# Kernel optimization log

Hardware: AMD Instinct MI355X
Metric: run time of the kernel (lower is better)

The kernel has to match this reference:

```python
import jax, jax.numpy as jnp
import numpy as np

EMBED_DIM = 1024
NUM_HEADS = 16
HEAD_DIM = EMBED_DIM // NUM_HEADS
B, S = 4, 2048


def setup_inputs() -> dict:
    key = jax.random.key(0)
    ks = jax.random.split(key, 9)
    s = 1.0 / np.sqrt(EMBED_DIM)
    x = jax.random.normal(ks[0], (B, S, EMBED_DIM), dtype=jnp.float32)
    # nn.Linear weights stored [out, in]; y = x @ W.T + b
    Wq = jax.random.uniform(ks[1], (EMBED_DIM, EMBED_DIM), jnp.float32, -s, s)
    bq = jax.random.uniform(ks[2], (EMBED_DIM,), jnp.float32, -s, s)
    Wk = jax.random.uniform(ks[3], (EMBED_DIM, EMBED_DIM), jnp.float32, -s, s)
    bk = jax.random.uniform(ks[4], (EMBED_DIM,), jnp.float32, -s, s)
    Wv = jax.random.uniform(ks[5], (EMBED_DIM, EMBED_DIM), jnp.float32, -s, s)
    bv = jax.random.uniform(ks[6], (EMBED_DIM,), jnp.float32, -s, s)
    Wo = jax.random.uniform(ks[7], (EMBED_DIM, EMBED_DIM), jnp.float32, -s, s)
    bo = jax.random.uniform(ks[8], (EMBED_DIM,), jnp.float32, -s, s)
    return {"x": x, "Wq": Wq, "bq": bq, "Wk": Wk, "bk": bk,
            "Wv": Wv, "bv": bv, "Wo": Wo, "bo": bo}


def _split_heads(t):
    b, s, _ = t.shape
    return t.reshape(b, s, NUM_HEADS, HEAD_DIM).transpose(0, 2, 1, 3)  # [B,H,S,D]


def reference(x, Wq, bq, Wk, bk, Wv, bv, Wo, bo):
    q = _split_heads(x @ Wq.T + bq)
    k = _split_heads(x @ Wk.T + bk)
    v = _split_heads(x @ Wv.T + bv)
    scores = jnp.einsum('bhqd,bhkd->bhqk', q, k) / np.sqrt(HEAD_DIM)  # [B,H,S,S]
    attn = jax.nn.softmax(scores, axis=-1)
    ctx = jnp.einsum('bhqk,bhkd->bhqd', attn, v)          # [B,H,S,D]
    ctx = ctx.transpose(0, 2, 1, 3).reshape(x.shape[0], x.shape[1], EMBED_DIM)
    return ctx @ Wo.T + bo
```

## Files before the change

### kernel.cpp

```cpp
#include <hip/hip_runtime.h>
#include <hip/hip_bf16.h>
#include <stdint.h>

typedef __attribute__((ext_vector_type(8))) short  bf16x8;
typedef __attribute__((ext_vector_type(4))) float  f32x4;

#define LOG2E 1.4426950408889634f

__device__ __forceinline__ unsigned short f2bf(float f) {
  unsigned int u = __builtin_bit_cast(unsigned int, f);
  u += 0x7fffu + ((u >> 16) & 1u);
  return (unsigned short)(u >> 16);
}

__device__ __forceinline__ unsigned int pk2(float a, float b) {
  __hip_bfloat162 h = __float22bfloat162_rn(make_float2(a, b));
  unsigned int u;
  __builtin_memcpy(&u, &h, 4);
  return u;
}

__device__ __forceinline__ void async16(const void* g, void* l) {
  __builtin_amdgcn_global_load_lds(
      (const __attribute__((address_space(1))) unsigned int*)g,
      (__attribute__((address_space(3))) unsigned int*)l,
      16, 0, 0);
}

__global__ __launch_bounds__(256) void cast_all(
    const float* __restrict__ x,
    const float* __restrict__ Wq, const float* __restrict__ Wk,
    const float* __restrict__ Wv, const float* __restrict__ Wo,
    unsigned short* __restrict__ xb, unsigned short* __restrict__ wqkv,
    unsigned short* __restrict__ wo) {
  int i = blockIdx.x * 256 + threadIdx.x;
  const float* src;
  unsigned short* dst;
  int off;
  if (i < 2097152) {
    src = x; dst = xb; off = i;
  } else {
    int j = i - 2097152;
    int seg = j >> 18; off = j & 262143;
    src = (seg == 0) ? Wq : (seg == 1) ? Wk : (seg == 2) ? Wv : Wo;
    dst = (seg < 3) ? (wqkv + (size_t)seg * 1048576) : wo;
  }
  float4 f = ((const float4*)src)[off];
  uint2 o;
  o.x = pk2(f.x, f.y);
  o.y = pk2(f.z, f.w);
  ((uint2*)dst)[off] = o;
}

__global__ __launch_bounds__(256) void gemm_qkv(
    const unsigned short* __restrict__ xb, const unsigned short* __restrict__ wqkv,
    const float* __restrict__ bq, const float* __restrict__ bk, const float* __restrict__ bv,
    unsigned short* __restrict__ qb, unsigned short* __restrict__ kb,
    unsigned short* __restrict__ vb) {
  __shared__ __align__(16) unsigned short As[128 * 32];
  __shared__ __align__(16) unsigned short Bs[128 * 32];
  __shared__ __align__(16) unsigned short epi[4][64 * 72];
  const int bid = blockIdx.x;
  const int xcd = bid & 7, idx = bid >> 3;
  const int nt = xcd * 3 + (idx % 3);
  const int mt = idx / 3;
  const int m0 = mt * 128, n0 = nt * 128;
  const int tid = threadIdx.x;
  const int wv = tid >> 6, lane = tid & 63, qq = lane >> 4, ln = lane & 15;
  const int wm = wv & 1, wn = wv >> 1;
  const int K = 1024;

  f32x4 acc[4][4];
#pragma unroll
  for (int i = 0; i < 4; ++i)
#pragma unroll
    for (int j = 0; j < 4; ++j) acc[i][j] = f32x4{0.f, 0.f, 0.f, 0.f};

  for (int k0 = 0; k0 < K; k0 += 32) {
#pragma unroll
    for (int i = 0; i < 2; ++i) {
      int cc = wv * 2 + i;
      int jp = cc * 64 + lane;
      int row = jp >> 2, cp = jp & 3;
      int c = cp ^ ((row >> 1) & 3);
      async16(xb   + (size_t)(m0 + row) * K + k0 + c * 8, As + cc * 512);
      async16(wqkv + (size_t)(n0 + row) * K + k0 + c * 8, Bs + cc * 512);
    }
    __syncthreads();
    bf16x8 af[4], bf[4];
#pragma unroll
    for (int i = 0; i < 4; ++i) {
      int row = wm * 64 + i * 16 + ln;
      af[i] = *(const bf16x8*)(As + row * 32 + (qq ^ ((row >> 1) & 3)) * 8);
    }
#pragma unroll
    for (int j = 0; j < 4; ++j) {
      int row = wn * 64 + j * 16 + ln;
      bf[j] = *(const bf16x8*)(Bs + row * 32 + (qq ^ ((row >> 1) & 3)) * 8);
    }
#pragma unroll
    for (int i = 0; i < 4; ++i)
#pragma unroll
      for (int j = 0; j < 4; ++j)
        acc[i][j] = __builtin_amdgcn_mfma_f32_16x16x32_bf16(af[i], bf[j], acc[i][j], 0, 0, 0);
    __syncthreads();
  }

  const int nblk = n0 >> 10;
  const float* bias = (nblk == 0) ? bq : (nblk == 1) ? bk : bv;
  const float scale = (nblk == 0) ? (0.125f * LOG2E) : 1.0f;
  unsigned short* buf = epi[wv];
  const int ncol0 = (n0 & 1023) + wn * 64;
  const int head  = ncol0 >> 6;
  const int mbase = m0 + wm * 64;
  const int b     = mbase >> 11, sbase = mbase & 2047;
  unsigned short* dst = (nblk == 0) ? qb : (nblk == 1) ? kb : vb;

  if (nblk != 2) {
#pragma unroll
    for (int j = 0; j < 4; ++j) {
      float bs = bias[ncol0 + j * 16 + ln] * scale;
#pragma unroll
      for (int i = 0; i < 4; ++i)
#pragma unroll
        for (int r = 0; r < 4; ++r)
          buf[(i * 16 + qq * 4 + r) * 72 + j * 16 + ln] = f2bf(acc[i][j][r] * scale + bs);
    }
    unsigned short* gout = dst + (((size_t)(b * 16 + head)) * 2048 + sbase) * 64;
#pragma unroll
    for (int h = 0; h < 2; ++h)
#pragma unroll
      for (int p = 0; p < 4; ++p) {
        int rr = (lane >> 2) + p * 16;
        int c4 = lane & 3;
        ulonglong2 v = *(const ulonglong2*)(buf + rr * 72 + h * 32 + c4 * 8);
        *(ulonglong2*)(gout + (size_t)rr * 64 + h * 32 + c4 * 8) = v;
      }
  } else {
#pragma unroll
    for (int j = 0; j < 4; ++j) {
      float bs = bias[ncol0 + j * 16 + ln];
#pragma unroll
      for (int i = 0; i < 4; ++i) {
        uint2 pk;
        pk.x = pk2(acc[i][j][0] + bs, acc[i][j][1] + bs);
        pk.y = pk2(acc[i][j][2] + bs, acc[i][j][3] + bs);
        *(uint2*)(buf + (j * 16 + ln) * 72 + i * 16 + qq * 4) = pk;
      }
    }
    unsigned short* gout = dst + ((size_t)(b * 16 + head)) * 64 * 2048 + sbase;
#pragma unroll
    for (int p = 0; p < 8; ++p) {
      int dr = (lane >> 3) + p * 8;
      int c8 = lane & 7;
      ulonglong2 v = *(const ulonglong2*)(buf + dr * 72 + c8 * 8);
      *(ulonglong2*)(gout + (size_t)dr * 2048 + c8 * 8) = v;
    }
  }
}

__global__ __launch_bounds__(256, 4) void attn_kernel(
    const unsigned short* __restrict__ qb, const unsigned short* __restrict__ kb,
    const unsigned short* __restrict__ vb, unsigned short* __restrict__ ctx) {
  __shared__ __align__(16) unsigned short k_sh[2][64 * 64];
  __shared__ __align__(16) unsigned short vT_sh[64 * 64];
  __shared__ __align__(16) unsigned short p_sh[128 * 64];
  const int bid = blockIdx.x;
  const int xcd = bid & 7, idx = bid >> 3;
  const int bh = xcd * 8 + (idx >> 4);
  const int q0 = (idx & 15) * 128;
  const int tid = threadIdx.x;
  const int wv = tid >> 6, lane = tid & 63, qq = lane >> 4, ln = lane & 15;

  bf16x8 qf[2][2];
  {
    const unsigned short* qbase = qb + ((size_t)bh * 2048 + q0 + wv * 32) * 64;
#pragma unroll
    for (int rb = 0; rb < 2; ++rb)
#pragma unroll
      for (int kq = 0; kq < 2; ++kq)
        qf[rb][kq] = *(const bf16x8*)(qbase + (rb * 16 + ln) * 64 + kq * 32 + qq * 8);
  }

  f32x4 o_acc[2][4];
  float l_i[2] = {0.f, 0.f};
#pragma unroll
  for (int rb = 0; rb < 2; ++rb)
#pragma unroll
    for (int nt = 0; nt < 4; ++nt) o_acc[rb][nt] = f32x4{0.f, 0.f, 0.f, 0.f};

  const unsigned short* kgbase = kb + (size_t)bh * 2048 * 64;
  const unsigned short* vgbase = vb + (size_t)bh * 64 * 2048;
  const int cc0 = wv * 2;

  auto stageK = [&](int kt, unsigned short* dst) {
#pragma unroll
    for (int i = 0; i < 2; ++i) {
      int jp = (cc0 + i) * 64 + lane;
      int row = jp >> 3, c = (jp & 7) ^ (row & 7);
      async16(kgbase + (size_t)(kt * 64 + row) * 64 + c * 8, dst + (cc0 + i) * 512);
    }
  };
  auto stageV = [&](int kt) {
#pragma unroll
    for (int i = 0; i < 2; ++i) {
      int jp = (cc0 + i) * 64 + lane;
      int row = jp >> 3, c = (jp & 7) ^ (row & 7);
      async16(vgbase + (size_t)row * 2048 + kt * 64 + c * 8, vT_sh + (cc0 + i) * 512);
    }
  };

  stageK(0, k_sh[0]);
  stageV(0);

  for (int kt = 0; kt < 32; ++kt) {
    const unsigned short* kcur = k_sh[kt & 1];
    if (kt < 31) {
      stageK(kt + 1, k_sh[(kt & 1) ^ 1]);
      asm volatile("s_waitcnt vmcnt(4)" ::: "memory");
    } else {
      asm volatile("s_waitcnt vmcnt(2)" ::: "memory");
    }
    __builtin_amdgcn_s_barrier();

    f32x4 s_acc[2][4];
#pragma unroll
    for (int rb = 0; rb < 2; ++rb)
#pragma unroll
      for (int ct = 0; ct < 4; ++ct) s_acc[rb][ct] = f32x4{0.f, 0.f, 0.f, 0.f};
    __builtin_amdgcn_s_setprio(1);
#pragma unroll
    for (int ct = 0; ct < 4; ++ct) {
      int row = ct * 16 + ln;
      bf16x8 kf0 = *(const bf16x8*)(kcur + row * 64 + ((0 + qq) ^ (row & 7)) * 8);
      bf16x8 kf1 = *(const bf16x8*)(kcur + row * 64 + ((4 + qq) ^ (row & 7)) * 8);
#pragma unroll
      for (int rb = 0; rb < 2; ++rb) {
        s_acc[rb][ct] = __builtin_amdgcn_mfma_f32_16x16x32_bf16(kf0, qf[rb][0], s_acc[rb][ct], 0, 0, 0);
        s_acc[rb][ct] = __builtin_amdgcn_mfma_f32_16x16x32_bf16(kf1, qf[rb][1], s_acc[rb][ct], 0, 0, 0);
      }
    }
    __builtin_amdgcn_s_setprio(0);

#pragma unroll
    for (int rb = 0; rb < 2; ++rb) {
      int prow = wv * 32 + rb * 16 + ln;
      int rs = prow & 7;
      float sum = 0.f;
#pragma unroll
      for (int ct = 0; ct < 4; ++ct) {
        float p0 = __builtin_amdgcn_exp2f(s_acc[rb][ct][0]);
        float p1 = __builtin_amdgcn_exp2f(s_acc[rb][ct][1]);
        float p2 = __builtin_amdgcn_exp2f(s_acc[rb][ct][2]);
        float p3 = __builtin_amdgcn_exp2f(s_acc[rb][ct][3]);
        sum += (p0 + p1) + (p2 + p3);
        uint2 pk;
        pk.x = pk2(p0, p1);
        pk.y = pk2(p2, p3);
        *(uint2*)(p_sh + prow * 64 + (((ct * 2 + (qq >> 1)) ^ rs) << 3) + ((qq & 1) << 2)) = pk;
      }
      l_i[rb] += sum;
    }

    if (kt < 31) asm volatile("s_waitcnt vmcnt(2)" ::: "memory");
    else         asm volatile("s_waitcnt vmcnt(0)" ::: "memory");
    __builtin_amdgcn_s_barrier();

#pragma unroll
    for (int kk = 0; kk < 2; ++kk) {
      bf16x8 vf[4], pf[2];
#pragma unroll
      for (int nt = 0; nt < 4; ++nt) {
        int row = nt * 16 + ln;
        vf[nt] = *(const bf16x8*)(vT_sh + row * 64 + ((kk * 4 + qq) ^ (row & 7)) * 8);
      }
#pragma unroll
      for (int rb = 0; rb < 2; ++rb) {
        int row = wv * 32 + rb * 16 + ln;
        pf[rb] = *(const bf16x8*)(p_sh + row * 64 + (((kk * 4 + qq) ^ (row & 7)) << 3));
      }
      __builtin_amdgcn_s_setprio(1);
#pragma unroll
      for (int rb = 0; rb < 2; ++rb)
#pragma unroll
        for (int nt = 0; nt < 4; ++nt)
          o_acc[rb][nt] = __builtin_amdgcn_mfma_f32_16x16x32_bf16(vf[nt], pf[rb], o_acc[rb][nt], 0, 0, 0);
      __builtin_amdgcn_s_setprio(0);
    }
    __builtin_amdgcn_s_barrier();
    if (kt < 31) stageV(kt + 1);
  }

#pragma unroll
  for (int rb = 0; rb < 2; ++rb) {
    l_i[rb] += __shfl_xor(l_i[rb], 16);
    l_i[rb] += __shfl_xor(l_i[rb], 32);
    float inv = 1.0f / l_i[rb];
    int row = wv * 32 + rb * 16 + ln;
    int rs = row & 7;
#pragma unroll
    for (int nt = 0; nt < 4; ++nt) {
      uint2 pk;
      pk.x = pk2(o_acc[rb][nt][0] * inv, o_acc[rb][nt][1] * inv);
      pk.y = pk2(o_acc[rb][nt][2] * inv, o_acc[rb][nt][3] * inv);
      *(uint2*)(p_sh + row * 64 + (((nt * 2 + (qq >> 1)) ^ rs) << 3) + ((qq & 1) << 2)) = pk;
    }
  }
  {
    const int b = bh >> 4, h = bh & 15;
    int r = tid >> 1, half = tid & 1;
    int rs = r & 7;
    int s = q0 + r;
    size_t gbase = ((size_t)(b * 2048 + s)) * 1024 + h * 64 + half * 32;
    const unsigned short* lsrc = p_sh + r * 64;
#pragma unroll
    for (int j = 0; j < 4; ++j)
      ((ulonglong2*)(ctx + gbase + j * 8))[0] =
          *(const ulonglong2*)(lsrc + (((half * 4 + j) ^ rs) << 3));
  }
}

__global__ __launch_bounds__(256) void gemm_out(
    const unsigned short* __restrict__ ctx, const unsigned short* __restrict__ wo,
    const float* __restrict__ bo, float* __restrict__ out) {
  __shared__ __align__(16) unsigned short As[2][128 * 32];
  __shared__ __align__(16) unsigned short Bs[2][128 * 32];
  const int bid = blockIdx.x;
  const int n0 = (bid & 7) * 128;
  const int m0 = (bid >> 3) * 128;
  const int tid = threadIdx.x;
  const int wv = tid >> 6, lane = tid & 63, qq = lane >> 4, ln = lane & 15;
  const int wm = wv & 1, wn = wv >> 1;
  const int K = 1024;

  f32x4 acc[4][4];
#pragma unroll
  for (int i = 0; i < 4; ++i)
#pragma unroll
    for (int j = 0; j < 4; ++j) acc[i][j] = f32x4{0.f, 0.f, 0.f, 0.f};

  auto stage = [&](int t, int buf) {
#pragma unroll
    for (int i = 0; i < 2; ++i) {
      int cc = wv * 2 + i;
      int jp = cc * 64 + lane;
      int row = jp >> 2, cp = jp & 3;
      int c = cp ^ ((row >> 1) & 3);
      async16(ctx + (size_t)(m0 + row) * K + t * 32 + c * 8, As[buf] + cc * 512);
      async16(wo  + (size_t)(n0 + row) * K + t * 32 + c * 8, Bs[buf] + cc * 512);
    }
  };

  stage(0, 0);
  for (int t = 0; t < 32; ++t) {
    const int cur = t & 1;
    if (t < 31) {
      stage(t + 1, cur ^ 1);
      asm volatile("s_waitcnt vmcnt(4)" ::: "memory");
    } else {
      asm volatile("s_waitcnt vmcnt(0)" ::: "memory");
    }
    __builtin_amdgcn_s_barrier();

    bf16x8 af[4], bf[4];
#pragma unroll
    for (int i = 0; i < 4; ++i) {
      int row = wm * 64 + i * 16 + ln;
      af[i] = *(const bf16x8*)(As[cur] + row * 32 + (qq ^ ((row >> 1) & 3)) * 8);
    }
#pragma unroll
    for (int j = 0; j < 4; ++j) {
      int row = wn * 64 + j * 16 + ln;
      bf[j] = *(const bf16x8*)(Bs[cur] + row * 32 + (qq ^ ((row >> 1) & 3)) * 8);
    }
#pragma unroll
    for (int i = 0; i < 4; ++i)
#pragma unroll
      for (int j = 0; j < 4; ++j)
        acc[i][j] = __builtin_amdgcn_mfma_f32_16x16x32_bf16(af[i], bf[j], acc[i][j], 0, 0, 0);
    __builtin_amdgcn_s_barrier();
  }

#pragma unroll
  for (int j = 0; j < 4; ++j) {
    int n = n0 + wn * 64 + j * 16 + ln;
    float bsv = bo[n];
#pragma unroll
    for (int i = 0; i < 4; ++i) {
#pragma unroll
      for (int r = 0; r < 4; ++r) {
        int m = m0 + wm * 64 + i * 16 + qq * 4 + r;
        out[(size_t)m * 1024 + n] = acc[i][j][r] + bsv;
      }
    }
  }
}

extern "C" void kernel_launch(void* const* d_in, const int* in_sizes, int n_in,
                              void* d_out, int out_size, void* d_ws, size_t ws_size,
                              hipStream_t stream) {
  const float* x  = (const float*)d_in[0];
  const float* Wq = (const float*)d_in[1];
  const float* bq = (const float*)d_in[2];
  const float* Wk = (const float*)d_in[3];
  const float* bk = (const float*)d_in[4];
  const float* Wv = (const float*)d_in[5];
  const float* bv = (const float*)d_in[6];
  const float* Wo = (const float*)d_in[7];
  const float* bo = (const float*)d_in[8];
  float* out = (float*)d_out;

  char* ws = (char*)d_ws;
  unsigned short* xb   = (unsigned short*)(ws);
  unsigned short* ctxb = (unsigned short*)(ws);
  unsigned short* qb   = (unsigned short*)(ws + ((size_t)16 << 20));
  unsigned short* kbuf = (unsigned short*)(ws + ((size_t)32 << 20));
  unsigned short* vbuf = (unsigned short*)(ws + ((size_t)48 << 20));
  unsigned short* wqkv = (unsigned short*)(ws + ((size_t)64 << 20));
  unsigned short* wo   = (unsigned short*)(ws + ((size_t)70 << 20));

  cast_all<<<12288, 256, 0, stream>>>(x, Wq, Wk, Wv, Wo, xb, wqkv, wo);

  gemm_qkv<<<1536, 256, 0, stream>>>(xb, wqkv, bq, bk, bv, qb, kbuf, vbuf);
  attn_kernel<<<1024, 256, 0, stream>>>(qb, kbuf, vbuf, ctxb);
  gemm_out<<<512, 256, 0, stream>>>(ctxb, wo, bo, out);
}
```

Baseline: 283.9 us.

## Keep P in registers via permlane swaps and double-buffer V with K

Instead of writing the softmax probabilities to shared memory and reading them back as MFMA operands, the attention kernel now rearranges the packed bf16 values across lanes with permlane32/permlane16 swaps, so P stays in registers. V is double-buffered alongside K and both are loaded in one staging call, which cuts the per-iteration barriers from three to one. LDS use shrinks (p_sh removed, K buffer reused for the epilogue), which may raise occupancy. The risks are lane-permutation correctness and a full vmcnt(0) wait at the end of each iteration, which may expose load latency.

```diff
diff --git a/kernel.cpp b/kernel.cpp
--- a/kernel.cpp
+++ b/kernel.cpp
@@ -4,6 +4,8 @@
 
 typedef __attribute__((ext_vector_type(8))) short  bf16x8;
 typedef __attribute__((ext_vector_type(4))) float  f32x4;
+typedef __attribute__((ext_vector_type(4))) unsigned int u32x4;
+typedef __attribute__((ext_vector_type(2))) unsigned int u32x2;
 
 #define LOG2E 1.4426950408889634f
 
@@ -163,8 +165,7 @@
     const unsigned short* __restrict__ qb, const unsigned short* __restrict__ kb,
     const unsigned short* __restrict__ vb, unsigned short* __restrict__ ctx) {
   __shared__ __align__(16) unsigned short k_sh[2][64 * 64];
-  __shared__ __align__(16) unsigned short vT_sh[64 * 64];
-  __shared__ __align__(16) unsigned short p_sh[128 * 64];
+  __shared__ __align__(16) unsigned short vT_sh[2][64 * 64];
   const int bid = blockIdx.x;
   const int xcd = bid & 7, idx = bid >> 3;
   const int bh = xcd * 8 + (idx >> 4);
@@ -193,35 +194,25 @@
   const unsigned short* vgbase = vb + (size_t)bh * 64 * 2048;
   const int cc0 = wv * 2;
 
-  auto stageK = [&](int kt, unsigned short* dst) {
+  auto stageKV = [&](int kt, int buf) {
 #pragma unroll
     for (int i = 0; i < 2; ++i) {
       int jp = (cc0 + i) * 64 + lane;
       int row = jp >> 3, c = (jp & 7) ^ (row & 7);
-      async16(kgbase + (size_t)(kt * 64 + row) * 64 + c * 8, dst + (cc0 + i) * 512);
+      async16(kgbase + (size_t)(kt * 64 + row) * 64 + c * 8, k_sh[buf] + (cc0 + i) * 512);
+      async16(vgbase + (size_t)row * 2048 + kt * 64 + c * 8, vT_sh[buf] + (cc0 + i) * 512);
     }
   };
-  auto stageV = [&](int kt) {
-#pragma unroll
-    for (int i = 0; i < 2; ++i) {
-      int jp = (cc0 + i) * 64 + lane;
-      int row = jp >> 3, c = (jp & 7) ^ (row & 7);
-      async16(vgbase + (size_t)row * 2048 + kt * 64 + c * 8, vT_sh + (cc0 + i) * 512);
-    }
-  };
-
-  stageK(0, k_sh[0]);
-  stageV(0);
+
+  stageKV(0, 0);
+  asm volatile("s_waitcnt vmcnt(0)" ::: "memory");
+  __builtin_amdgcn_s_barrier();
 
   for (int kt = 0; kt < 32; ++kt) {
-    const unsigned short* kcur = k_sh[kt & 1];
-    if (kt < 31) {
-      stageK(kt + 1, k_sh[(kt & 1) ^ 1]);
-      asm volatile("s_waitcnt vmcnt(4)" ::: "memory");
-    } else {
-      asm volatile("s_waitcnt vmcnt(2)" ::: "memory");
-    }
-    __builtin_amdgcn_s_barrier();
+    const int cur = kt & 1;
+    const unsigned short* kcur = k_sh[cur];
+    const unsigned short* vcur = vT_sh[cur];
+    if (kt < 31) stageKV(kt + 1, cur ^ 1);
 
     f32x4 s_acc[2][4];
 #pragma unroll
@@ -242,10 +233,10 @@
     }
     __builtin_amdgcn_s_setprio(0);
 
+    bf16x8 pf[2][2];
 #pragma unroll
     for (int rb = 0; rb < 2; ++rb) {
-      int prow = wv * 32 + rb * 16 + ln;
-      int rs = prow & 7;
+      unsigned int W[4][2];
       float sum = 0.f;
 #pragma unroll
       for (int ct = 0; ct < 4; ++ct) {
@@ -254,43 +245,43 @@
         float p2 = __builtin_amdgcn_exp2f(s_acc[rb][ct][2]);
         float p3 = __builtin_amdgcn_exp2f(s_acc[rb][ct][3]);
         sum += (p0 + p1) + (p2 + p3);
-        uint2 pk;
-        pk.x = pk2(p0, p1);
-        pk.y = pk2(p2, p3);
-        *(uint2*)(p_sh + prow * 64 + (((ct * 2 + (qq >> 1)) ^ rs) << 3) + ((qq & 1) << 2)) = pk;
+        W[ct][0] = pk2(p0, p1);
+        W[ct][1] = pk2(p2, p3);
       }
       l_i[rb] += sum;
-    }
-
-    if (kt < 31) asm volatile("s_waitcnt vmcnt(2)" ::: "memory");
-    else         asm volatile("s_waitcnt vmcnt(0)" ::: "memory");
-    __builtin_amdgcn_s_barrier();
+#pragma unroll
+      for (int kk = 0; kk < 2; ++kk) {
+        u32x2 a1 = __builtin_amdgcn_permlane32_swap(W[2 * kk][0], W[2 * kk + 1][0], false, false);
+        u32x2 a2 = __builtin_amdgcn_permlane16_swap(a1.x, a1.y, false, false);
+        u32x2 b1 = __builtin_amdgcn_permlane32_swap(W[2 * kk][1], W[2 * kk + 1][1], false, false);
+        u32x2 b2 = __builtin_amdgcn_permlane16_swap(b1.x, b1.y, false, false);
+        u32x4 pw = {a2.x, b2.x, a2.y, b2.y};
+        pf[rb][kk] = __builtin_bit_cast(bf16x8, pw);
+      }
+    }
 
 #pragma unroll
     for (int kk = 0; kk < 2; ++kk) {
-      bf16x8 vf[4], pf[2];
+      bf16x8 vf[4];
 #pragma unroll
       for (int nt = 0; nt < 4; ++nt) {
         int row = nt * 16 + ln;
-        vf[nt] = *(const bf16x8*)(vT_sh + row * 64 + ((kk * 4 + qq) ^ (row & 7)) * 8);
-      }
-#pragma unroll
-      for (int rb = 0; rb < 2; ++rb) {
-        int row = wv * 32 + rb * 16 + ln;
-        pf[rb] = *(const bf16x8*)(p_sh + row * 64 + (((kk * 4 + qq) ^ (row & 7)) << 3));
+        vf[nt] = *(const bf16x8*)(vcur + row * 64 + ((kk * 4 + qq) ^ (row & 7)) * 8);
       }
       __builtin_amdgcn_s_setprio(1);
 #pragma unroll
       for (int rb = 0; rb < 2; ++rb)
 #pragma unroll
         for (int nt = 0; nt < 4; ++nt)
-          o_acc[rb][nt] = __builtin_amdgcn_mfma_f32_16x16x32_bf16(vf[nt], pf[rb], o_acc[rb][nt], 0, 0, 0);
+          o_acc[rb][nt] = __builtin_amdgcn_mfma_f32_16x16x32_bf16(vf[nt], pf[rb][kk], o_acc[rb][nt], 0, 0, 0);
       __builtin_amdgcn_s_setprio(0);
     }
+
+    if (kt < 31) asm volatile("s_waitcnt vmcnt(0)" ::: "memory");
     __builtin_amdgcn_s_barrier();
-    if (kt < 31) stageV(kt + 1);
-  }
-
+  }
+
+  unsigned short* ep = (unsigned short*)k_sh;
 #pragma unroll
   for (int rb = 0; rb < 2; ++rb) {
     l_i[rb] += __shfl_xor(l_i[rb], 16);
@@ -303,7 +294,7 @@
       uint2 pk;
       pk.x = pk2(o_acc[rb][nt][0] * inv, o_acc[rb][nt][1] * inv);
       pk.y = pk2(o_acc[rb][nt][2] * inv, o_acc[rb][nt][3] * inv);
-      *(uint2*)(p_sh + row * 64 + (((nt * 2 + (qq >> 1)) ^ rs) << 3) + ((qq & 1) << 2)) = pk;
+      *(uint2*)(ep + row * 64 + (((nt * 2 + (qq >> 1)) ^ rs) << 3) + ((qq & 1) << 2)) = pk;
     }
   }
   {
@@ -312,7 +303,7 @@
     int rs = r & 7;
     int s = q0 + r;
     size_t gbase = ((size_t)(b * 2048 + s)) * 1024 + h * 64 + half * 32;
-    const unsigned short* lsrc = p_sh + r * 64;
+    const unsigned short* lsrc = ep + r * 64;
 #pragma unroll
     for (int j = 0; j < 4; ++j)
       ((ulonglong2*)(ctx + gbase + j * 8))[0] =
```

After: 297.6 us. 1.05x slower.
